# Performance work log

Measured on AMD Instinct MI355X. Metric: run time of the kernel, lower is better.

Reference implementation:

```python
import jax, jax.numpy as jnp
import numpy as np

NEG_SLOPE = 0.2


def add_self_loops(edge_index, num_nodes):
    loop = jnp.arange(num_nodes, dtype=edge_index.dtype)
    src = jnp.concatenate([edge_index[0], loop])
    dst = jnp.concatenate([edge_index[1], loop])
    return src, dst


def gat_conv(x, src, dst, W, att_src, att_dst, bias, heads, out_ch, concat):
    N = x.shape[0]
    h = (x @ W).reshape(N, heads, out_ch)                      # [N,H,C]
    a_src = jnp.sum(h * att_src, axis=-1)                      # [N,H]
    a_dst = jnp.sum(h * att_dst, axis=-1)                      # [N,H]
    e = a_src[src] + a_dst[dst]                                # [E,H]
    e = jax.nn.leaky_relu(e, NEG_SLOPE)
    # segment softmax over incoming edges of each destination node
    m = jax.ops.segment_max(e, dst, num_segments=N)            # [N,H]
    m = jnp.where(jnp.isfinite(m), m, 0.0)
    ex = jnp.exp(e - m[dst])
    s = jax.ops.segment_sum(ex, dst, num_segments=N)           # [N,H]
    alpha = ex / jnp.where(s[dst] > 0, s[dst], 1.0)            # [E,H]
    msg = alpha[:, :, None] * h[src]                           # [E,H,C]
    out = jax.ops.segment_sum(msg, dst, num_segments=N)        # [N,H,C]
    if concat:
        out = out.reshape(N, heads * out_ch)
    else:
        out = out.mean(axis=1)
    return out + bias


def setup_inputs() -> dict:
    key = jax.random.key(0)
    ks = jax.random.split(key, 10)
    N, F, E, H, C1 = 50000, 128, 800000, 8, 8
    x = jax.random.normal(ks[0], (N, F), dtype=jnp.float32)
    edge_index = jax.random.randint(ks[1], (2, E), 0, N, dtype=jnp.int64)
    sc = 0.1
    W1 = jax.random.normal(ks[2], (F, H * C1), dtype=jnp.float32) * sc
    a_src1 = jax.random.normal(ks[3], (H, C1), dtype=jnp.float32) * sc
    a_dst1 = jax.random.normal(ks[4], (H, C1), dtype=jnp.float32) * sc
    b1 = jnp.zeros((H * C1,), dtype=jnp.float32)
    W2 = jax.random.normal(ks[5], (H * C1, F), dtype=jnp.float32) * sc
    a_src2 = jax.random.normal(ks[6], (1, F), dtype=jnp.float32) * sc
    a_dst2 = jax.random.normal(ks[7], (1, F), dtype=jnp.float32) * sc
    b2 = jnp.zeros((F,), dtype=jnp.float32)
    return {"x": x, "edge_index": edge_index, "W1": W1, "a_src1": a_src1,
            "a_dst1": a_dst1, "b1": b1, "W2": W2, "a_src2": a_src2,
            "a_dst2": a_dst2, "b2": b2}


def reference(x, edge_index, W1, a_src1, a_dst1, b1, W2, a_src2, a_dst2, b2):
    N = x.shape[0]
    src, dst = add_self_loops(edge_index, N)
    h = gat_conv(x, src, dst, W1, a_src1, a_dst1, b1, heads=8, out_ch=8, concat=True)
    h = jax.nn.elu(h)
    out = gat_conv(h, src, dst, W2, a_src2, a_dst2, b2, heads=1, out_ch=x.shape[1], concat=True)
    return out
```

## Files before the change

### kernel.cpp

```cpp
#include <hip/hip_runtime.h>
#include <hip/hip_fp16.h>
#include <math.h>

#define NEG_SLOPE 0.2f
#define BSTRIDE 6144

typedef _Float16 f16x8 __attribute__((ext_vector_type(8)));
typedef float    f32x4 __attribute__((ext_vector_type(4)));

__device__ __forceinline__ void get_edge(const int* __restrict__ ei, int E, int e,
                                         int& s, int& d) {
    if (e < E) { s = ei[e]; d = ei[E + e]; }
    else       { s = e - E; d = e - E; }
}

__global__ __launch_bounds__(256) void bucket_scatter(const int* __restrict__ ei, int E, int ET,
                                                      int* __restrict__ bcur,
                                                      unsigned int* __restrict__ bstore,
                                                      int nbuck) {
    __shared__ int lhist[256], lbase[256], lrank[256], gbase[256];
    __shared__ unsigned int sbuf[4096];
    __shared__ int saddr[4096];
    int t = threadIdx.x;
    int start = blockIdx.x * 4096;
    int cnt = ET - start; if (cnt > 4096) cnt = 4096;
    lhist[t] = 0; lrank[t] = 0;
    __syncthreads();
    int mybuck[16]; unsigned int myval[16];
#pragma unroll
    for (int k = 0; k < 16; ++k) {
        int e = start + t + k * 256;
        mybuck[k] = -1;
        if (e < ET) {
            int s, d; get_edge(ei, E, e, s, d);
            mybuck[k] = d >> 8;
            myval[k] = ((unsigned int)d << 16) | (unsigned int)s;
            atomicAdd(&lhist[mybuck[k]], 1);
        }
    }
    __syncthreads();
    int v = lhist[t];
    lbase[t] = v;
    __syncthreads();
    for (int off = 1; off < 256; off <<= 1) {
        int u = (t >= off) ? lbase[t - off] : 0;
        __syncthreads();
        lbase[t] += u;
        __syncthreads();
    }
    int excl = lbase[t] - v;
    if (t < nbuck && v > 0) gbase[t] = atomicAdd(&bcur[t], v);
    __syncthreads();
    lbase[t] = excl;
    __syncthreads();
#pragma unroll
    for (int k = 0; k < 16; ++k) {
        int b = mybuck[k];
        if (b >= 0) {
            int r = atomicAdd(&lrank[b], 1);
            int idx = lbase[b] + r;
            sbuf[idx] = myval[k];
            saddr[idx] = gbase[b] + r;
        }
    }
    __syncthreads();
    for (int j = t; j < cnt; j += 256)
        bstore[saddr[j]] = sbuf[j];
}

__global__ __launch_bounds__(256) void bucket_csr64(const unsigned int* __restrict__ bstore,
                                                    const int* __restrict__ bcur,
                                                    int* __restrict__ cnt,
                                                    int* __restrict__ col, int N) {
    __shared__ int lrank[256];
    int b = blockIdx.x, t = threadIdx.x;
    int base = b * BSTRIDE;
    int nb = bcur[b] - base;
    lrank[t] = 0;
    __syncthreads();
    for (int i = t; i < nb; i += 256) {
        unsigned int pk = bstore[base + i];
        int local = (pk >> 16) & 255;
        int r = atomicAdd(&lrank[local], 1);
        if (r < 64) col[(((b << 8) + local) << 6) + r] = (int)(pk & 0xFFFFu);
    }
    __syncthreads();
    int node = (b << 8) + t;
    if (node < N) cnt[node] = lrank[t];
}

__global__ __launch_bounds__(256) void gemm1_kernel(const float* __restrict__ x,
                                                    const float* __restrict__ W,
                                                    const float* __restrict__ asrc,
                                                    const float* __restrict__ adst,
                                                    _Float16* __restrict__ hout,
                                                    float* __restrict__ av,
                                                    float* __restrict__ bv, int N,
                                                    int gblocks,
                                                    const float* __restrict__ W2,
                                                    const float* __restrict__ as2,
                                                    const float* __restrict__ ad2,
                                                    float* __restrict__ wa,
                                                    float* __restrict__ wb,
                                                    int* __restrict__ bcur) {
    if (blockIdx.x == (unsigned)gblocks) {
        int k = threadIdx.x;
        bcur[k] = k * BSTRIDE;
        if (k < 64) {
            const float* wr = W2 + k * 128;
            float sa = 0.f, sb = 0.f;
#pragma unroll 8
            for (int c = 0; c < 128; ++c) {
                float w = wr[c];
                sa = fmaf(w, as2[c], sa);
                sb = fmaf(w, ad2[c], sb);
            }
            wa[k] = sa; wb[k] = sb;
        }
        return;
    }
    __shared__ unsigned int sWu[4096];
    for (int p = threadIdx.x; p < 4096; p += 256) {
        int frag = p >> 8;
        int lane = (p >> 2) & 63;
        int j2   = p & 3;
        int chunk = frag >> 2, nt = frag & 3;
        int k = chunk * 32 + ((lane >> 4) << 3) + (j2 << 1);
        int n = nt * 16 + (lane & 15);
        union { _Float16 h[2]; unsigned int u; } pk;
        pk.h[0] = (_Float16)W[k * 64 + n];
        pk.h[1] = (_Float16)W[(k + 1) * 64 + n];
        sWu[p] = pk.u;
    }
    __syncthreads();

    int lane = threadIdx.x & 63;
    int wid  = threadIdx.x >> 6;
    int rbase = blockIdx.x * 64 + wid * 16;
    int l15 = lane & 15, quad = lane >> 4;
    int rA = rbase + l15; if (rA >= N) rA = N - 1;

    const unsigned int* fragbase = &sWu[lane * 4];
    f32x4 z = {0.f, 0.f, 0.f, 0.f};
    f32x4 acc[4] = {z, z, z, z};

#pragma unroll
    for (int chunk = 0; chunk < 4; ++chunk) {
        const float* xp = x + (size_t)rA * 128 + chunk * 32 + quad * 8;
        float4 f0 = *((const float4*)xp);
        float4 f1 = *((const float4*)(xp + 4));
        f16x8 af;
        af[0] = (_Float16)f0.x; af[1] = (_Float16)f0.y;
        af[2] = (_Float16)f0.z; af[3] = (_Float16)f0.w;
        af[4] = (_Float16)f1.x; af[5] = (_Float16)f1.y;
        af[6] = (_Float16)f1.z; af[7] = (_Float16)f1.w;
#pragma unroll
        for (int t = 0; t < 4; ++t) {
            f16x8 bf = *((const f16x8*)(fragbase + (chunk * 4 + t) * 256));
            acc[t] = __builtin_amdgcn_mfma_f32_16x16x32_f16(af, bf, acc[t], 0, 0, 0);
        }
    }

    float asc[4], adc[4];
#pragma unroll
    for (int t = 0; t < 4; ++t) { asc[t] = asrc[t * 16 + l15]; adc[t] = adst[t * 16 + l15]; }
#pragma unroll
    for (int reg = 0; reg < 4; ++reg) {
        int r = rbase + quad * 4 + reg;
        bool ok = (r < N);
#pragma unroll
        for (int t = 0; t < 4; ++t) {
            float v = acc[t][reg];
            if (ok) hout[(size_t)r * 64 + t * 16 + l15] = (_Float16)v;
            float pa = v * asc[t], pb = v * adc[t];
            pa += __shfl_xor(pa, 1); pb += __shfl_xor(pb, 1);
            pa += __shfl_xor(pa, 2); pb += __shfl_xor(pb, 2);
            pa += __shfl_xor(pa, 4); pb += __shfl_xor(pb, 4);
            if (ok && (lane & 7) == 0) {
                int head = t * 2 + (l15 >> 3);
                av[r * 8 + head] = pa;
                bv[r * 8 + head] = pb;
            }
        }
    }
}

__global__ __launch_bounds__(512) void agg1_kernel(const int* __restrict__ cnt,
                                                   const int* __restrict__ col,
                                                   const float* __restrict__ av,
                                                   const float* __restrict__ bv,
                                                   const __half* __restrict__ h1,
                                                   const float* __restrict__ b1,
                                                   const float* __restrict__ wa,
                                                   const float* __restrict__ wb,
                                                   _Float16* __restrict__ out1,
                                                   float* __restrict__ av2,
                                                   float* __restrict__ bv2, int N) {
    int lane = threadIdx.x & 63;
    int node = blockIdx.x * 16 + (threadIdx.x >> 6) * 2 + (lane >> 5);
    bool valid = node < N;
    int nodeC = valid ? node : N - 1;
    int g  = (lane >> 3) & 3;
    int gl = lane & 7;
    int beg = nodeC << 6;
    int deg = cnt[nodeC]; if (deg > 64) deg = 64;
    int end = beg + deg;
    int last = end - 1;
    float bd = bv[nodeC * 8 + gl];
    const uint4* hrow = (const uint4*)h1;

    uint4 z4 = {0u, 0u, 0u, 0u};
    int e = beg + g;
    int c0 = col[e      <= last ? e      : last];
    int c1 = col[e + 4  <= last ? e + 4  : last];
    int c2 = col[e + 8  <= last ? e + 8  : last];
    float av0 = 0.f, av1v = 0.f; uint4 h0 = z4, h1v = z4;
    if (e < end)     { av0  = av[c0 * 8 + gl]; h0  = hrow[(size_t)c0 * 8 + gl]; }
    if (e + 4 < end) { av1v = av[c1 * 8 + gl]; h1v = hrow[(size_t)c1 * 8 + gl]; }

    float s = 0.f, a0 = 0.f, a1 = 0.f, a2 = 0.f, a3 = 0.f,
          a4 = 0.f, a5 = 0.f, a6 = 0.f, a7 = 0.f;
    for (; e < end; e += 4) {
        float av2v = 0.f; uint4 h2 = z4;
        if (e + 8 < end) { av2v = av[c2 * 8 + gl]; h2 = hrow[(size_t)c2 * 8 + gl]; }
        int c3 = col[e + 12 <= last ? e + 12 : last];
        float l = av0 + bd;
        l = l > 0.f ? l : NEG_SLOPE * l;
        float w = __expf(l);
        float2 f0 = __half22float2(*(const __half2*)&h0.x);
        float2 f1 = __half22float2(*(const __half2*)&h0.y);
        float2 f2 = __half22float2(*(const __half2*)&h0.z);
        float2 f3 = __half22float2(*(const __half2*)&h0.w);
        s += w;
        a0 = fmaf(w, f0.x, a0); a1 = fmaf(w, f0.y, a1);
        a2 = fmaf(w, f1.x, a2); a3 = fmaf(w, f1.y, a3);
        a4 = fmaf(w, f2.x, a4); a5 = fmaf(w, f2.y, a5);
        a6 = fmaf(w, f3.x, a6); a7 = fmaf(w, f3.y, a7);
        av0 = av1v; h0 = h1v; av1v = av2v; h1v = h2; c2 = c3;
    }
#pragma unroll
    for (int off = 8; off < 32; off <<= 1) {
        s  += __shfl_xor(s, off);
        a0 += __shfl_xor(a0, off); a1 += __shfl_xor(a1, off);
        a2 += __shfl_xor(a2, off); a3 += __shfl_xor(a3, off);
        a4 += __shfl_xor(a4, off); a5 += __shfl_xor(a5, off);
        a6 += __shfl_xor(a6, off); a7 += __shfl_xor(a7, off);
    }
    float inv = __builtin_amdgcn_rcpf(s);
    float4 bb0 = ((const float4*)b1)[gl * 2];
    float4 bb1 = ((const float4*)b1)[gl * 2 + 1];
    float v0 = a0 * inv + bb0.x, v1 = a1 * inv + bb0.y;
    float v2 = a2 * inv + bb0.z, v3 = a3 * inv + bb0.w;
    float v4 = a4 * inv + bb1.x, v5 = a5 * inv + bb1.y;
    float v6 = a6 * inv + bb1.z, v7 = a7 * inv + bb1.w;
    v0 = v0 > 0.f ? v0 : __expf(v0) - 1.f; v1 = v1 > 0.f ? v1 : __expf(v1) - 1.f;
    v2 = v2 > 0.f ? v2 : __expf(v2) - 1.f; v3 = v3 > 0.f ? v3 : __expf(v3) - 1.f;
    v4 = v4 > 0.f ? v4 : __expf(v4) - 1.f; v5 = v5 > 0.f ? v5 : __expf(v5) - 1.f;
    v6 = v6 > 0.f ? v6 : __expf(v6) - 1.f; v7 = v7 > 0.f ? v7 : __expf(v7) - 1.f;
    float4 wa0 = ((const float4*)wa)[gl * 2], wa1 = ((const float4*)wa)[gl * 2 + 1];
    float4 wb0 = ((const float4*)wb)[gl * 2], wb1 = ((const float4*)wb)[gl * 2 + 1];
    float pa = v0 * wa0.x + v1 * wa0.y + v2 * wa0.z + v3 * wa0.w
             + v4 * wa1.x + v5 * wa1.y + v6 * wa1.z + v7 * wa1.w;
    float pb = v0 * wb0.x + v1 * wb0.y + v2 * wb0.z + v3 * wb0.w
             + v4 * wb1.x + v5 * wb1.y + v6 * wb1.z + v7 * wb1.w;
    pa += __shfl_xor(pa, 1); pb += __shfl_xor(pb, 1);
    pa += __shfl_xor(pa, 2); pb += __shfl_xor(pb, 2);
    pa += __shfl_xor(pa, 4); pb += __shfl_xor(pb, 4);
    if (valid && (lane & 31) == 0) { av2[node] = pa; bv2[node] = pb; }
    if (valid && g == 0) {
        f16x8 o;
        o[0] = (_Float16)v0; o[1] = (_Float16)v1; o[2] = (_Float16)v2; o[3] = (_Float16)v3;
        o[4] = (_Float16)v4; o[5] = (_Float16)v5; o[6] = (_Float16)v6; o[7] = (_Float16)v7;
        ((f16x8*)out1)[(size_t)node * 8 + gl] = o;
    }
}

__global__ __launch_bounds__(512) void agg2_kernel(const int* __restrict__ cnt,
                                                   const int* __restrict__ col,
                                                   const float* __restrict__ av,
                                                   const float* __restrict__ bv,
                                                   const __half* __restrict__ out1,
                                                   _Float16* __restrict__ agg64, int N) {
    int lane = threadIdx.x & 63;
    int node = blockIdx.x * 16 + (threadIdx.x >> 6) * 2 + (lane >> 5);
    bool valid = node < N;
    int nodeC = valid ? node : N - 1;
    int g  = (lane >> 3) & 3;
    int gl = lane & 7;
    int beg = nodeC << 6;
    int deg = cnt[nodeC]; if (deg > 64) deg = 64;
    int end = beg + deg;
    int last = end - 1;
    float bd = bv[nodeC];
    const uint4* hrow = (const uint4*)out1;

    uint4 z4 = {0u, 0u, 0u, 0u};
    int e = beg + g;
    int c0 = col[e      <= last ? e      : last];
    int c1 = col[e + 4  <= last ? e + 4  : last];
    int c2 = col[e + 8  <= last ? e + 8  : last];
    float av0 = 0.f, av1v = 0.f; uint4 h0 = z4, h1v = z4;
    if (e < end)     { av0  = av[c0]; h0  = hrow[(size_t)c0 * 8 + gl]; }
    if (e + 4 < end) { av1v = av[c1]; h1v = hrow[(size_t)c1 * 8 + gl]; }

    float s = 0.f, a0 = 0.f, a1 = 0.f, a2 = 0.f, a3 = 0.f,
          a4 = 0.f, a5 = 0.f, a6 = 0.f, a7 = 0.f;
    for (; e < end; e += 4) {
        float av2v = 0.f; uint4 h2 = z4;
        if (e + 8 < end) { av2v = av[c2]; h2 = hrow[(size_t)c2 * 8 + gl]; }
        int c3 = col[e + 12 <= last ? e + 12 : last];
        float l = av0 + bd;
        l = l > 0.f ? l : NEG_SLOPE * l;
        float w = __expf(l);
        float2 f0 = __half22float2(*(const __half2*)&h0.x);
        float2 f1 = __half22float2(*(const __half2*)&h0.y);
        float2 f2 = __half22float2(*(const __half2*)&h0.z);
        float2 f3 = __half22float2(*(const __half2*)&h0.w);
        s += w;
        a0 = fmaf(w, f0.x, a0); a1 = fmaf(w, f0.y, a1);
        a2 = fmaf(w, f1.x, a2); a3 = fmaf(w, f1.y, a3);
        a4 = fmaf(w, f2.x, a4); a5 = fmaf(w, f2.y, a5);
        a6 = fmaf(w, f3.x, a6); a7 = fmaf(w, f3.y, a7);
        av0 = av1v; h0 = h1v; av1v = av2v; h1v = h2; c2 = c3;
    }
#pragma unroll
    for (int off = 8; off < 32; off <<= 1) {
        s  += __shfl_xor(s, off);
        a0 += __shfl_xor(a0, off); a1 += __shfl_xor(a1, off);
        a2 += __shfl_xor(a2, off); a3 += __shfl_xor(a3, off);
        a4 += __shfl_xor(a4, off); a5 += __shfl_xor(a5, off);
        a6 += __shfl_xor(a6, off); a7 += __shfl_xor(a7, off);
    }
    if (valid && g == 0) {
        float inv = __builtin_amdgcn_rcpf(s);
        f16x8 o;
        o[0] = (_Float16)(a0 * inv); o[1] = (_Float16)(a1 * inv);
        o[2] = (_Float16)(a2 * inv); o[3] = (_Float16)(a3 * inv);
        o[4] = (_Float16)(a4 * inv); o[5] = (_Float16)(a5 * inv);
        o[6] = (_Float16)(a6 * inv); o[7] = (_Float16)(a7 * inv);
        ((f16x8*)agg64)[(size_t)node * 8 + gl] = o;
    }
}

__global__ __launch_bounds__(256) void gemm2_kernel(const _Float16* __restrict__ he,
                                                    const float* __restrict__ W,
                                                    const float* __restrict__ b2,
                                                    float* __restrict__ dout, int N) {
    __shared__ unsigned int sWu[4096];
    for (int p = threadIdx.x; p < 4096; p += 256) {
        int frag = p >> 8;
        int lane = (p >> 2) & 63;
        int j2   = p & 3;
        int chunk = frag >> 3, nt = frag & 7;
        int k = chunk * 32 + ((lane >> 4) << 3) + (j2 << 1);
        int n = nt * 16 + (lane & 15);
        union { _Float16 h[2]; unsigned int u; } pk;
        pk.h[0] = (_Float16)W[k * 128 + n];
        pk.h[1] = (_Float16)W[(k + 1) * 128 + n];
        sWu[p] = pk.u;
    }
    __syncthreads();

    int lane = threadIdx.x & 63;
    int wid  = threadIdx.x >> 6;
    int rbase = blockIdx.x * 64 + wid * 16;
    int l15 = lane & 15, quad = lane >> 4;
    int rA = rbase + l15; if (rA >= N) rA = N - 1;

    const unsigned int* fragbase = &sWu[lane * 4];
    f32x4 z = {0.f, 0.f, 0.f, 0.f};
    f32x4 acc[8] = {z, z, z, z, z, z, z, z};

#pragma unroll
    for (int chunk = 0; chunk < 2; ++chunk) {
        const _Float16* xp = he + (size_t)rA * 64 + chunk * 32 + quad * 8;
        f16x8 af = *((const f16x8*)xp);
#pragma unroll
        for (int t = 0; t < 8; ++t) {
            f16x8 bf = *((const f16x8*)(fragbase + (chunk * 8 + t) * 256));
            acc[t] = __builtin_amdgcn_mfma_f32_16x16x32_f16(af, bf, acc[t], 0, 0, 0);
        }
    }

    float bcol[8];
#pragma unroll
    for (int t = 0; t < 8; ++t) bcol[t] = b2[t * 16 + l15];
#pragma unroll
    for (int reg = 0; reg < 4; ++reg) {
        int r = rbase + quad * 4 + reg;
        if (r < N) {
#pragma unroll
            for (int t = 0; t < 8; ++t)
                dout[(size_t)r * 128 + t * 16 + l15] = acc[t][reg] + bcol[t];
        }
    }
}

extern "C" void kernel_launch(void* const* d_in, const int* in_sizes, int n_in,
                              void* d_out, int out_size, void* d_ws, size_t ws_size,
                              hipStream_t stream) {
    const float* x      = (const float*)d_in[0];
    const int*   ei     = (const int*)  d_in[1];
    const float* W1     = (const float*)d_in[2];
    const float* a_src1 = (const float*)d_in[3];
    const float* a_dst1 = (const float*)d_in[4];
    const float* b1     = (const float*)d_in[5];
    const float* W2     = (const float*)d_in[6];
    const float* a_src2 = (const float*)d_in[7];
    const float* a_dst2 = (const float*)d_in[8];
    const float* b2     = (const float*)d_in[9];
    float* dout = (float*)d_out;

    const int N  = in_sizes[0] / 128;
    const int E  = in_sizes[1] / 2;
    const int ET = E + N;
    const int NBUCK = (N + 255) >> 8;
    const int NBLKA = (ET + 4095) >> 12;

    char* wsb = (char*)d_ws;
    _Float16* h1     = (_Float16*)wsb; wsb += (size_t)N * 64 * 2;
    _Float16* out1   = (_Float16*)wsb; wsb += (size_t)N * 64 * 2;
    _Float16* agg64h = (_Float16*)wsb; wsb += (size_t)N * 64 * 2;
    float* av1  = (float*)wsb; wsb += (size_t)N * 8 * 4;
    float* bv1  = (float*)wsb; wsb += (size_t)N * 8 * 4;
    float* av2  = (float*)wsb; wsb += (size_t)N * 4;
    float* bv2  = (float*)wsb; wsb += (size_t)N * 4;
    float* wa   = (float*)wsb; wsb += 64 * 4;
    float* wb   = (float*)wsb; wsb += 64 * 4;
    int* cnt    = (int*)wsb; wsb += (size_t)N * 4;
    int* col    = (int*)wsb; wsb += (size_t)N * 64 * 4;
    unsigned int* bstore = (unsigned int*)wsb; wsb += (size_t)NBUCK * BSTRIDE * 4;
    int* bcur   = (int*)wsb; wsb += 256 * 4;

    const int B = 256;
    const int gblocks = (N + 63) / 64;

    gemm1_kernel<<<gblocks + 1, B, 0, stream>>>(x, W1, a_src1, a_dst1, h1, av1, bv1, N,
                                                gblocks, W2, a_src2, a_dst2, wa, wb, bcur);

    bucket_scatter<<<NBLKA, B, 0, stream>>>(ei, E, ET, bcur, bstore, NBUCK);
    bucket_csr64<<<NBUCK, B, 0, stream>>>(bstore, bcur, cnt, col, N);

    agg1_kernel<<<(N + 15) / 16, 512, 0, stream>>>(cnt, col, av1, bv1,
                                                   (const __half*)h1, b1, wa, wb,
                                                   out1, av2, bv2, N);

    agg2_kernel<<<(N + 15) / 16, 512, 0, stream>>>(cnt, col, av2, bv2,
                                                   (const __half*)out1, agg64h, N);
    gemm2_kernel<<<gblocks, B, 0, stream>>>(agg64h, W2, b2, dout, N);
}
```

Measured before the change: 185.5 us.

## Fuse gemm1 with bucket scatter, fuse agg2 with gemm2, narrow col to u16

Merges the first GEMM and the edge bucket-scatter into one launch, with block roles chosen by block index and a shared-memory union. The per-bucket counter now starts at zero via a memset and offsets are added inside the kernel. The second aggregation and second GEMM are fused: aggregated rows stay in LDS and feed the MFMA directly, so the N×64 fp16 intermediate is never written to or read from global memory. Column indices are stored as 16-bit values, halving index traffic; this relies on N fitting in 16 bits. The trade-offs are an extra memset launch and fused kernels that use more LDS and serialise four aggregation passes per block.

```diff
diff --git a/kernel.cpp b/kernel.cpp
--- a/kernel.cpp
+++ b/kernel.cpp
@@ -14,100 +14,38 @@
     else       { s = e - E; d = e - E; }
 }
 
-__global__ __launch_bounds__(256) void bucket_scatter(const int* __restrict__ ei, int E, int ET,
-                                                      int* __restrict__ bcur,
-                                                      unsigned int* __restrict__ bstore,
-                                                      int nbuck) {
-    __shared__ int lhist[256], lbase[256], lrank[256], gbase[256];
-    __shared__ unsigned int sbuf[4096];
-    __shared__ int saddr[4096];
+union G1SMem {
+    unsigned int sWu[4096];
+    struct {
+        int lhist[256], lbase[256], lrank[256], gbase[256];
+        unsigned int sbuf[4096];
+        int saddr[4096];
+    } sc;
+};
+
+__global__ __launch_bounds__(256) void g1s_kernel(const float* __restrict__ x,
+                                                  const float* __restrict__ W,
+                                                  const float* __restrict__ asrc,
+                                                  const float* __restrict__ adst,
+                                                  _Float16* __restrict__ hout,
+                                                  float* __restrict__ av,
+                                                  float* __restrict__ bv, int N,
+                                                  int gblocks,
+                                                  const float* __restrict__ W2,
+                                                  const float* __restrict__ as2,
+                                                  const float* __restrict__ ad2,
+                                                  float* __restrict__ wa,
+                                                  float* __restrict__ wb,
+                                                  int* __restrict__ bcur,
+                                                  const int* __restrict__ ei, int E, int ET,
+                                                  unsigned int* __restrict__ bstore,
+                                                  int nbuck) {
+    __shared__ G1SMem sm;
     int t = threadIdx.x;
-    int start = blockIdx.x * 4096;
-    int cnt = ET - start; if (cnt > 4096) cnt = 4096;
-    lhist[t] = 0; lrank[t] = 0;
-    __syncthreads();
-    int mybuck[16]; unsigned int myval[16];
-#pragma unroll
-    for (int k = 0; k < 16; ++k) {
-        int e = start + t + k * 256;
-        mybuck[k] = -1;
-        if (e < ET) {
-            int s, d; get_edge(ei, E, e, s, d);
-            mybuck[k] = d >> 8;
-            myval[k] = ((unsigned int)d << 16) | (unsigned int)s;
-            atomicAdd(&lhist[mybuck[k]], 1);
-        }
-    }
-    __syncthreads();
-    int v = lhist[t];
-    lbase[t] = v;
-    __syncthreads();
-    for (int off = 1; off < 256; off <<= 1) {
-        int u = (t >= off) ? lbase[t - off] : 0;
-        __syncthreads();
-        lbase[t] += u;
-        __syncthreads();
-    }
-    int excl = lbase[t] - v;
-    if (t < nbuck && v > 0) gbase[t] = atomicAdd(&bcur[t], v);
-    __syncthreads();
-    lbase[t] = excl;
-    __syncthreads();
-#pragma unroll
-    for (int k = 0; k < 16; ++k) {
-        int b = mybuck[k];
-        if (b >= 0) {
-            int r = atomicAdd(&lrank[b], 1);
-            int idx = lbase[b] + r;
-            sbuf[idx] = myval[k];
-            saddr[idx] = gbase[b] + r;
-        }
-    }
-    __syncthreads();
-    for (int j = t; j < cnt; j += 256)
-        bstore[saddr[j]] = sbuf[j];
-}
-
-__global__ __launch_bounds__(256) void bucket_csr64(const unsigned int* __restrict__ bstore,
-                                                    const int* __restrict__ bcur,
-                                                    int* __restrict__ cnt,
-                                                    int* __restrict__ col, int N) {
-    __shared__ int lrank[256];
-    int b = blockIdx.x, t = threadIdx.x;
-    int base = b * BSTRIDE;
-    int nb = bcur[b] - base;
-    lrank[t] = 0;
-    __syncthreads();
-    for (int i = t; i < nb; i += 256) {
-        unsigned int pk = bstore[base + i];
-        int local = (pk >> 16) & 255;
-        int r = atomicAdd(&lrank[local], 1);
-        if (r < 64) col[(((b << 8) + local) << 6) + r] = (int)(pk & 0xFFFFu);
-    }
-    __syncthreads();
-    int node = (b << 8) + t;
-    if (node < N) cnt[node] = lrank[t];
-}
-
-__global__ __launch_bounds__(256) void gemm1_kernel(const float* __restrict__ x,
-                                                    const float* __restrict__ W,
-                                                    const float* __restrict__ asrc,
-                                                    const float* __restrict__ adst,
-                                                    _Float16* __restrict__ hout,
-                                                    float* __restrict__ av,
-                                                    float* __restrict__ bv, int N,
-                                                    int gblocks,
-                                                    const float* __restrict__ W2,
-                                                    const float* __restrict__ as2,
-                                                    const float* __restrict__ ad2,
-                                                    float* __restrict__ wa,
-                                                    float* __restrict__ wb,
-                                                    int* __restrict__ bcur) {
+
     if (blockIdx.x == (unsigned)gblocks) {
-        int k = threadIdx.x;
-        bcur[k] = k * BSTRIDE;
-        if (k < 64) {
-            const float* wr = W2 + k * 128;
+        if (t < 64) {
+            const float* wr = W2 + t * 128;
             float sa = 0.f, sb = 0.f;
 #pragma unroll 8
             for (int c = 0; c < 128; ++c) {
@@ -115,12 +53,62 @@
                 sa = fmaf(w, as2[c], sa);
                 sb = fmaf(w, ad2[c], sb);
             }
-            wa[k] = sa; wb[k] = sb;
+            wa[t] = sa; wb[t] = sb;
         }
         return;
     }
-    __shared__ unsigned int sWu[4096];
-    for (int p = threadIdx.x; p < 4096; p += 256) {
+
+    if (blockIdx.x > (unsigned)gblocks) {
+        int sblk = blockIdx.x - gblocks - 1;
+        int start = sblk * 4096;
+        int cnt = ET - start; if (cnt > 4096) cnt = 4096;
+        sm.sc.lhist[t] = 0; sm.sc.lrank[t] = 0;
+        __syncthreads();
+        int mybuck[16]; unsigned int myval[16];
+#pragma unroll
+        for (int k = 0; k < 16; ++k) {
+            int e = start + t + k * 256;
+            mybuck[k] = -1;
+            if (e < ET) {
+                int s, d; get_edge(ei, E, e, s, d);
+                mybuck[k] = d >> 8;
+                myval[k] = ((unsigned int)d << 16) | (unsigned int)s;
+                atomicAdd(&sm.sc.lhist[mybuck[k]], 1);
+            }
+        }
+        __syncthreads();
+        int v = sm.sc.lhist[t];
+        sm.sc.lbase[t] = v;
+        __syncthreads();
+        for (int off = 1; off < 256; off <<= 1) {
+            int u = (t >= off) ? sm.sc.lbase[t - off] : 0;
+            __syncthreads();
+            sm.sc.lbase[t] += u;
+            __syncthreads();
+        }
+        int excl = sm.sc.lbase[t] - v;
+        if (t < nbuck && v > 0)
+            sm.sc.gbase[t] = t * BSTRIDE + atomicAdd(&bcur[t], v);
+        __syncthreads();
+        sm.sc.lbase[t] = excl;
+        __syncthreads();
+#pragma unroll
+        for (int k = 0; k < 16; ++k) {
+            int b = mybuck[k];
+            if (b >= 0) {
+                int r = atomicAdd(&sm.sc.lrank[b], 1);
+                int idx = sm.sc.lbase[b] + r;
+                sm.sc.sbuf[idx] = myval[k];
+                sm.sc.saddr[idx] = sm.sc.gbase[b] + r;
+            }
+        }
+        __syncthreads();
+        for (int j = t; j < cnt; j += 256)
+            bstore[sm.sc.saddr[j]] = sm.sc.sbuf[j];
+        return;
+    }
+
+    for (int p = t; p < 4096; p += 256) {
         int frag = p >> 8;
         int lane = (p >> 2) & 63;
         int j2   = p & 3;
@@ -130,17 +118,17 @@
         union { _Float16 h[2]; unsigned int u; } pk;
         pk.h[0] = (_Float16)W[k * 64 + n];
         pk.h[1] = (_Float16)W[(k + 1) * 64 + n];
-        sWu[p] = pk.u;
+        sm.sWu[p] = pk.u;
     }
     __syncthreads();
 
-    int lane = threadIdx.x & 63;
-    int wid  = threadIdx.x >> 6;
+    int lane = t & 63;
+    int wid  = t >> 6;
     int rbase = blockIdx.x * 64 + wid * 16;
     int l15 = lane & 15, quad = lane >> 4;
     int rA = rbase + l15; if (rA >= N) rA = N - 1;
 
-    const unsigned int* fragbase = &sWu[lane * 4];
+    const unsigned int* fragbase = &sm.sWu[lane * 4];
     f32x4 z = {0.f, 0.f, 0.f, 0.f};
     f32x4 acc[4] = {z, z, z, z};
 
@@ -155,29 +143,29 @@
         af[4] = (_Float16)f1.x; af[5] = (_Float16)f1.y;
         af[6] = (_Float16)f1.z; af[7] = (_Float16)f1.w;
 #pragma unroll
-        for (int t = 0; t < 4; ++t) {
-            f16x8 bf = *((const f16x8*)(fragbase + (chunk * 4 + t) * 256));
-            acc[t] = __builtin_amdgcn_mfma_f32_16x16x32_f16(af, bf, acc[t], 0, 0, 0);
+        for (int tt = 0; tt < 4; ++tt) {
+            f16x8 bf = *((const f16x8*)(fragbase + (chunk * 4 + tt) * 256));
+            acc[tt] = __builtin_amdgcn_mfma_f32_16x16x32_f16(af, bf, acc[tt], 0, 0, 0);
         }
     }
 
     float asc[4], adc[4];
 #pragma unroll
-    for (int t = 0; t < 4; ++t) { asc[t] = asrc[t * 16 + l15]; adc[t] = adst[t * 16 + l15]; }
+    for (int tt = 0; tt < 4; ++tt) { asc[tt] = asrc[tt * 16 + l15]; adc[tt] = adst[tt * 16 + l15]; }
 #pragma unroll
     for (int reg = 0; reg < 4; ++reg) {
         int r = rbase + quad * 4 + reg;
         bool ok = (r < N);
 #pragma unroll
-        for (int t = 0; t < 4; ++t) {
-            float v = acc[t][reg];
-            if (ok) hout[(size_t)r * 64 + t * 16 + l15] = (_Float16)v;
-            float pa = v * asc[t], pb = v * adc[t];
+        for (int tt = 0; tt < 4; ++tt) {
+            float v = acc[tt][reg];
+            if (ok) hout[(size_t)r * 64 + tt * 16 + l15] = (_Float16)v;
+            float pa = v * asc[tt], pb = v * adc[tt];
             pa += __shfl_xor(pa, 1); pb += __shfl_xor(pb, 1);
             pa += __shfl_xor(pa, 2); pb += __shfl_xor(pb, 2);
             pa += __shfl_xor(pa, 4); pb += __shfl_xor(pb, 4);
             if (ok && (lane & 7) == 0) {
-                int head = t * 2 + (l15 >> 3);
+                int head = tt * 2 + (l15 >> 3);
                 av[r * 8 + head] = pa;
                 bv[r * 8 + head] = pb;
             }
@@ -185,8 +173,29 @@
     }
 }
 
+__global__ __launch_bounds__(256) void bucket_csr64(const unsigned int* __restrict__ bstore,
+                                                    const int* __restrict__ bcur,
+                                                    int* __restrict__ cnt,
+                                                    unsigned short* __restrict__ col, int N) {
+    __shared__ int lrank[256];
+    int b = blockIdx.x, t = threadIdx.x;
+    int base = b * BSTRIDE;
+    int nb = bcur[b];
+    lrank[t] = 0;
+    __syncthreads();
+    for (int i = t; i < nb; i += 256) {
+        unsigned int pk = bstore[base + i];
+        int local = (pk >> 16) & 255;
+        int r = atomicAdd(&lrank[local], 1);
+        if (r < 64) col[(((b << 8) + local) << 6) + r] = (unsigned short)(pk & 0xFFFFu);
+    }
+    __syncthreads();
+    int node = (b << 8) + t;
+    if (node < N) cnt[node] = lrank[t];
+}
+
 __global__ __launch_bounds__(512) void agg1_kernel(const int* __restrict__ cnt,
-                                                   const int* __restrict__ col,
+                                                   const unsigned short* __restrict__ col,
                                                    const float* __restrict__ av,
                                                    const float* __restrict__ bv,
                                                    const __half* __restrict__ h1,
@@ -275,123 +284,126 @@
     }
 }
 
-__global__ __launch_bounds__(512) void agg2_kernel(const int* __restrict__ cnt,
-                                                   const int* __restrict__ col,
-                                                   const float* __restrict__ av,
-                                                   const float* __restrict__ bv,
-                                                   const __half* __restrict__ out1,
-                                                   _Float16* __restrict__ agg64, int N) {
-    int lane = threadIdx.x & 63;
-    int node = blockIdx.x * 16 + (threadIdx.x >> 6) * 2 + (lane >> 5);
-    bool valid = node < N;
-    int nodeC = valid ? node : N - 1;
-    int g  = (lane >> 3) & 3;
-    int gl = lane & 7;
-    int beg = nodeC << 6;
-    int deg = cnt[nodeC]; if (deg > 64) deg = 64;
-    int end = beg + deg;
-    int last = end - 1;
-    float bd = bv[nodeC];
-    const uint4* hrow = (const uint4*)out1;
-
-    uint4 z4 = {0u, 0u, 0u, 0u};
-    int e = beg + g;
-    int c0 = col[e      <= last ? e      : last];
-    int c1 = col[e + 4  <= last ? e + 4  : last];
-    int c2 = col[e + 8  <= last ? e + 8  : last];
-    float av0 = 0.f, av1v = 0.f; uint4 h0 = z4, h1v = z4;
-    if (e < end)     { av0  = av[c0]; h0  = hrow[(size_t)c0 * 8 + gl]; }
-    if (e + 4 < end) { av1v = av[c1]; h1v = hrow[(size_t)c1 * 8 + gl]; }
-
-    float s = 0.f, a0 = 0.f, a1 = 0.f, a2 = 0.f, a3 = 0.f,
-          a4 = 0.f, a5 = 0.f, a6 = 0.f, a7 = 0.f;
-    for (; e < end; e += 4) {
-        float av2v = 0.f; uint4 h2 = z4;
-        if (e + 8 < end) { av2v = av[c2]; h2 = hrow[(size_t)c2 * 8 + gl]; }
-        int c3 = col[e + 12 <= last ? e + 12 : last];
-        float l = av0 + bd;
-        l = l > 0.f ? l : NEG_SLOPE * l;
-        float w = __expf(l);
-        float2 f0 = __half22float2(*(const __half2*)&h0.x);
-        float2 f1 = __half22float2(*(const __half2*)&h0.y);
-        float2 f2 = __half22float2(*(const __half2*)&h0.z);
-        float2 f3 = __half22float2(*(const __half2*)&h0.w);
-        s += w;
-        a0 = fmaf(w, f0.x, a0); a1 = fmaf(w, f0.y, a1);
-        a2 = fmaf(w, f1.x, a2); a3 = fmaf(w, f1.y, a3);
-        a4 = fmaf(w, f2.x, a4); a5 = fmaf(w, f2.y, a5);
-        a6 = fmaf(w, f3.x, a6); a7 = fmaf(w, f3.y, a7);
-        av0 = av1v; h0 = h1v; av1v = av2v; h1v = h2; c2 = c3;
-    }
-#pragma unroll
-    for (int off = 8; off < 32; off <<= 1) {
-        s  += __shfl_xor(s, off);
-        a0 += __shfl_xor(a0, off); a1 += __shfl_xor(a1, off);
-        a2 += __shfl_xor(a2, off); a3 += __shfl_xor(a3, off);
-        a4 += __shfl_xor(a4, off); a5 += __shfl_xor(a5, off);
-        a6 += __shfl_xor(a6, off); a7 += __shfl_xor(a7, off);
-    }
-    if (valid && g == 0) {
-        float inv = __builtin_amdgcn_rcpf(s);
-        f16x8 o;
-        o[0] = (_Float16)(a0 * inv); o[1] = (_Float16)(a1 * inv);
-        o[2] = (_Float16)(a2 * inv); o[3] = (_Float16)(a3 * inv);
-        o[4] = (_Float16)(a4 * inv); o[5] = (_Float16)(a5 * inv);
-        o[6] = (_Float16)(a6 * inv); o[7] = (_Float16)(a7 * inv);
-        ((f16x8*)agg64)[(size_t)node * 8 + gl] = o;
-    }
-}
-
-__global__ __launch_bounds__(256) void gemm2_kernel(const _Float16* __restrict__ he,
-                                                    const float* __restrict__ W,
-                                                    const float* __restrict__ b2,
-                                                    float* __restrict__ dout, int N) {
+__global__ __launch_bounds__(512) void agg2g2_kernel(const int* __restrict__ cnt,
+                                                     const unsigned short* __restrict__ col,
+                                                     const float* __restrict__ av,
+                                                     const float* __restrict__ bv,
+                                                     const __half* __restrict__ out1,
+                                                     const float* __restrict__ W,
+                                                     const float* __restrict__ b2,
+                                                     float* __restrict__ dout, int N) {
     __shared__ unsigned int sWu[4096];
-    for (int p = threadIdx.x; p < 4096; p += 256) {
+    __shared__ _Float16 sAgg[64][72];
+    int t = threadIdx.x;
+    int lane = t & 63;
+    int wid  = t >> 6;
+    int rbase = blockIdx.x * 64;
+
+    for (int p = t; p < 4096; p += 512) {
         int frag = p >> 8;
-        int lane = (p >> 2) & 63;
-        int j2   = p & 3;
+        int ln = (p >> 2) & 63;
+        int j2 = p & 3;
         int chunk = frag >> 3, nt = frag & 7;
-        int k = chunk * 32 + ((lane >> 4) << 3) + (j2 << 1);
-        int n = nt * 16 + (lane & 15);
+        int k = chunk * 32 + ((ln >> 4) << 3) + (j2 << 1);
+        int n = nt * 16 + (ln & 15);
         union { _Float16 h[2]; unsigned int u; } pk;
         pk.h[0] = (_Float16)W[k * 128 + n];
         pk.h[1] = (_Float16)W[(k + 1) * 128 + n];
         sWu[p] = pk.u;
     }
+
+    int g  = (lane >> 3) & 3;
+    int gl = lane & 7;
+    const uint4* hrow = (const uint4*)out1;
+    uint4 z4 = {0u, 0u, 0u, 0u};
+#pragma unroll 1
+    for (int pass = 0; pass < 4; ++pass) {
+        int nl = pass * 16 + wid * 2 + (lane >> 5);
+        int node = rbase + nl;
+        bool valid = node < N;
+        int nodeC = valid ? node : N - 1;
+        int beg = nodeC << 6;
+        int deg = cnt[nodeC]; if (deg > 64) deg = 64;
+        int end = beg + deg;
+        int last = end - 1;
+        float bd = bv[nodeC];
+
+        int e = beg + g;
+        int c0 = col[e      <= last ? e      : last];
+        int c1 = col[e + 4  <= last ? e + 4  : last];
+        int c2 = col[e + 8  <= last ? e + 8  : last];
+        float av0 = 0.f, av1v = 0.f; uint4 h0 = z4, h1v = z4;
+        if (e < end)     { av0  = av[c0]; h0  = hrow[(size_t)c0 * 8 + gl]; }
+        if (e + 4 < end) { av1v = av[c1]; h1v = hrow[(size_t)c1 * 8 + gl]; }
+
+        float s = 0.f, a0 = 0.f, a1 = 0.f, a2 = 0.f, a3 = 0.f,
+              a4 = 0.f, a5 = 0.f, a6 = 0.f, a7 = 0.f;
+        for (; e < end; e += 4) {
+            float av2v = 0.f; uint4 h2 = z4;
+            if (e + 8 < end) { av2v = av[c2]; h2 = hrow[(size_t)c2 * 8 + gl]; }
+            int c3 = col[e + 12 <= last ? e + 12 : last];
+            float l = av0 + bd;
+            l = l > 0.f ? l : NEG_SLOPE * l;
+            float w = __expf(l);
+            float2 f0 = __half22float2(*(const __half2*)&h0.x);
+            float2 f1 = __half22float2(*(const __half2*)&h0.y);
+            float2 f2 = __half22float2(*(const __half2*)&h0.z);
+            float2 f3 = __half22float2(*(const __half2*)&h0.w);
+            s += w;
+            a0 = fmaf(w, f0.x, a0); a1 = fmaf(w, f0.y, a1);
+            a2 = fmaf(w, f1.x, a2); a3 = fmaf(w, f1.y, a3);
+            a4 = fmaf(w, f2.x, a4); a5 = fmaf(w, f2.y, a5);
+            a6 = fmaf(w, f3.x, a6); a7 = fmaf(w, f3.y, a7);
+            av0 = av1v; h0 = h1v; av1v = av2v; h1v = h2; c2 = c3;
+        }
+#pragma unroll
+        for (int off = 8; off < 32; off <<= 1) {
+            s  += __shfl_xor(s, off);
+            a0 += __shfl_xor(a0, off); a1 += __shfl_xor(a1, off);
+            a2 += __shfl_xor(a2, off); a3 += __shfl_xor(a3, off);
+            a4 += __shfl_xor(a4, off); a5 += __shfl_xor(a5, off);
+            a6 += __shfl_xor(a6, off); a7 += __shfl_xor(a7, off);
+        }
+        if (g == 0) {
+            float inv = __builtin_amdgcn_rcpf(s);
+            f16x8 o;
+            o[0] = (_Float16)(a0 * inv); o[1] = (_Float16)(a1 * inv);
+            o[2] = (_Float16)(a2 * inv); o[3] = (_Float16)(a3 * inv);
+            o[4] = (_Float16)(a4 * inv); o[5] = (_Float16)(a5 * inv);
+            o[6] = (_Float16)(a6 * inv); o[7] = (_Float16)(a7 * inv);
+            *((f16x8*)&sAgg[nl][gl * 8]) = o;
+        }
+    }
     __syncthreads();
 
-    int lane = threadIdx.x & 63;
-    int wid  = threadIdx.x >> 6;
-    int rbase = blockIdx.x * 64 + wid * 16;
+    int rblk = (wid & 3) * 16;
+    int chalf = wid >> 2;
     int l15 = lane & 15, quad = lane >> 4;
-    int rA = rbase + l15; if (rA >= N) rA = N - 1;
 
     const unsigned int* fragbase = &sWu[lane * 4];
     f32x4 z = {0.f, 0.f, 0.f, 0.f};
-    f32x4 acc[8] = {z, z, z, z, z, z, z, z};
+    f32x4 acc[4] = {z, z, z, z};
 
 #pragma unroll
     for (int chunk = 0; chunk < 2; ++chunk) {
-        const _Float16* xp = he + (size_t)rA * 64 + chunk * 32 + quad * 8;
-        f16x8 af = *((const f16x8*)xp);
-#pragma unroll
-        for (int t = 0; t < 8; ++t) {
-            f16x8 bf = *((const f16x8*)(fragbase + (chunk * 8 + t) * 256));
-            acc[t] = __builtin_amdgcn_mfma_f32_16x16x32_f16(af, bf, acc[t], 0, 0, 0);
-        }
-    }
-
-    float bcol[8];
-#pragma unroll
-    for (int t = 0; t < 8; ++t) bcol[t] = b2[t * 16 + l15];
+        f16x8 af = *((const f16x8*)&sAgg[rblk + l15][chunk * 32 + quad * 8]);
+#pragma unroll
+        for (int tt = 0; tt < 4; ++tt) {
+            f16x8 bf = *((const f16x8*)(fragbase + (chunk * 8 + chalf * 4 + tt) * 256));
+            acc[tt] = __builtin_amdgcn_mfma_f32_16x16x32_f16(af, bf, acc[tt], 0, 0, 0);
+        }
+    }
+
+    float bcol[4];
+#pragma unroll
+    for (int tt = 0; tt < 4; ++tt) bcol[tt] = b2[chalf * 64 + tt * 16 + l15];
 #pragma unroll
     for (int reg = 0; reg < 4; ++reg) {
-        int r = rbase + quad * 4 + reg;
+        int r = rbase + rblk + quad * 4 + reg;
         if (r < N) {
 #pragma unroll
-            for (int t = 0; t < 8; ++t)
-                dout[(size_t)r * 128 + t * 16 + l15] = acc[t][reg] + bcol[t];
+            for (int tt = 0; tt < 4; ++tt)
+                dout[(size_t)r * 128 + chalf * 64 + tt * 16 + l15] = acc[tt][reg] + bcol[tt];
         }
     }
 }
@@ -420,7 +432,6 @@
     char* wsb = (char*)d_ws;
     _Float16* h1     = (_Float16*)wsb; wsb += (size_t)N * 64 * 2;
     _Float16* out1   = (_Float16*)wsb; wsb += (size_t)N * 64 * 2;
-    _Float16* agg64h = (_Float16*)wsb; wsb += (size_t)N * 64 * 2;
     float* av1  = (float*)wsb; wsb += (size_t)N * 8 * 4;
     float* bv1  = (float*)wsb; wsb += (size_t)N * 8 * 4;
     float* av2  = (float*)wsb; wsb += (size_t)N * 4;
@@ -428,24 +439,25 @@
     float* wa   = (float*)wsb; wsb += 64 * 4;
     float* wb   = (float*)wsb; wsb += 64 * 4;
     int* cnt    = (int*)wsb; wsb += (size_t)N * 4;
-    int* col    = (int*)wsb; wsb += (size_t)N * 64 * 4;
+    unsigned short* col = (unsigned short*)wsb; wsb += (size_t)N * 64 * 2;
     unsigned int* bstore = (unsigned int*)wsb; wsb += (size_t)NBUCK * BSTRIDE * 4;
     int* bcur   = (int*)wsb; wsb += 256 * 4;
 
     const int B = 256;
     const int gblocks = (N + 63) / 64;
 
-    gemm1_kernel<<<gblocks + 1, B, 0, stream>>>(x, W1, a_src1, a_dst1, h1, av1, bv1, N,
-                                                gblocks, W2, a_src2, a_dst2, wa, wb, bcur);
-
-    bucket_scatter<<<NBLKA, B, 0, stream>>>(ei, E, ET, bcur, bstore, NBUCK);
+    hipMemsetAsync(bcur, 0, 256 * sizeof(int), stream);
+
+    g1s_kernel<<<gblocks + 1 + NBLKA, B, 0, stream>>>(x, W1, a_src1, a_dst1, h1, av1, bv1, N,
+                                                      gblocks, W2, a_src2, a_dst2, wa, wb,
+                                                      bcur, ei, E, ET, bstore, NBUCK);
+
     bucket_csr64<<<NBUCK, B, 0, stream>>>(bstore, bcur, cnt, col, N);
 
     agg1_kernel<<<(N + 15) / 16, 512, 0, stream>>>(cnt, col, av1, bv1,
                                                    (const __half*)h1, b1, wa, wb,
                                                    out1, av2, bv2, N);
 
-    agg2_kernel<<<(N + 15) / 16, 512, 0, stream>>>(cnt, col, av2, bv2,
-                                                   (const __half*)out1, agg64h, N);
-    gemm2_kernel<<<gblocks, B, 0, stream>>>(agg64h, W2, b2, dout, N);
-}
+    agg2g2_kernel<<<gblocks, 512, 0, stream>>>(cnt, col, av2, bv2,
+                                               (const __half*)out1, W2, b2, dout, N);
+}
```

Result: faster. 175.0 us (-5.7%).
